# Kernel tuning notes

Measured on AMD Instinct MI355X. Metric: run time of the kernel, lower is better.

## Reference

```python
import jax, jax.numpy as jnp
import numpy as np

NEG_INF_SCALE = -1e9


def setup_inputs() -> dict:
    key = jax.random.key(0)
    ks = jax.random.split(key, 8)
    B, T, M, D = 64, 1024, 256, 1024
    query = jax.random.normal(ks[0], (B, 1, M), dtype=jnp.float32)
    keys = jax.random.normal(ks[1], (B, T, M), dtype=jnp.float32)
    values = jax.random.normal(ks[2], (B, T, D), dtype=jnp.float32)
    mask = jax.random.randint(ks[3], (B, 1, T), 0, 2).astype(jnp.float32)
    # MLP params (scaled like torch default init ~ 1/sqrt(fan_in))
    W1 = jax.random.normal(ks[4], (4 * M, D), dtype=jnp.float32) / np.sqrt(4 * M)
    b1 = jnp.zeros((D,), dtype=jnp.float32)
    W2 = jax.random.normal(ks[5], (D, D), dtype=jnp.float32) / np.sqrt(D)
    b2 = jnp.zeros((D,), dtype=jnp.float32)
    w_score = jax.random.normal(ks[6], (D, 1), dtype=jnp.float32) / np.sqrt(D)
    b_score = jnp.zeros((1,), dtype=jnp.float32)
    return {"query": query, "keys": keys, "values": values, "mask": mask,
            "W1": W1, "b1": b1, "W2": W2, "b2": b2,
            "w_score": w_score, "b_score": b_score}


def reference(query, keys, values, mask, W1, b1, W2, b2, w_score, b_score):
    # query: [B,1,M] broadcast against keys: [B,T,M]
    q = jnp.broadcast_to(query, keys.shape)
    att_input = jnp.concatenate([q, keys, q - keys, q * keys], axis=-1)  # [B,T,4M]
    h = jax.nn.relu(att_input @ W1 + b1)   # [B,T,D]
    h = jax.nn.relu(h @ W2 + b2)           # [B,T,D]
    score = h @ w_score + b_score          # [B,T,1]
    logits = jnp.swapaxes(score, 1, 2)     # [B,1,T]
    logits = logits + mask * NEG_INF_SCALE
    attn = jax.nn.softmax(logits, axis=-1)  # [B,1,T]
    out = jnp.matmul(attn, values)          # [B,1,D]
    return out
```

## Files before the change

### kernel.cpp

```cpp
#include <hip/hip_runtime.h>

#define DEV __device__ __forceinline__

typedef __attribute__((ext_vector_type(4))) float f32x4;
typedef __attribute__((ext_vector_type(8))) short short8;
typedef __attribute__((ext_vector_type(4))) short s16x4;
typedef __attribute__((ext_vector_type(4))) float f32x4v;

DEV short f2bf(float f) {
  union { float f; unsigned u; } v; v.f = f;
  unsigned r = (v.u + 0x7FFFu + ((v.u >> 16) & 1u)) >> 16;
  return (short)r;
}

DEV void gload16(const void* g, void* l) {
  __builtin_amdgcn_global_load_lds(
      (const __attribute__((address_space(1))) void*)g,
      (__attribute__((address_space(3))) void*)l, 16, 0, 0);
}

#define BAR() __builtin_amdgcn_s_barrier()
#define LGKM0()                                          \
  {                                                      \
    asm volatile("s_waitcnt lgkmcnt(0)" ::: "memory");   \
    __builtin_amdgcn_sched_barrier(0);                   \
  }
#define VMW(n)                                                \
  {                                                           \
    asm volatile("s_waitcnt vmcnt(" #n ")" ::: "memory");     \
    __builtin_amdgcn_sched_barrier(0);                        \
  }

#define RD_A(pb, qrt)                                                          \
  _Pragma("unroll") for (int m_ = 0; m_ < 4; ++m_) {                           \
    af[m_][0] = *(const short8*)&lds[(pb) + aoff0 + ((qrt) * 4 + m_) * 1024];  \
    af[m_][1] = *(const short8*)&lds[(pb) + aoff1 + ((qrt) * 4 + m_) * 1024];  \
  }
#define RD_B(pb, nh)                                                             \
  _Pragma("unroll") for (int n_ = 0; n_ < 2; ++n_) {                             \
    bf[nh][n_][0] = *(const short8*)&lds[(pb) + boff0 + ((nh) * 2 + n_) * 1024]; \
    bf[nh][n_][1] = *(const short8*)&lds[(pb) + boff1 + ((nh) * 2 + n_) * 1024]; \
  }
#define MFMA_Q(mq, nh)                                                           \
  __builtin_amdgcn_s_setprio(1);                                                 \
  _Pragma("unroll") for (int m_ = 0; m_ < 4; ++m_) {                             \
    _Pragma("unroll") for (int n_ = 0; n_ < 2; ++n_) {                           \
      acc[(mq) * 4 + m_][(nh) * 2 + n_] =                                        \
          __builtin_amdgcn_mfma_f32_16x16x32_bf16(                               \
              af[m_][0], bf[nh][n_][0], acc[(mq) * 4 + m_][(nh) * 2 + n_], 0, 0, \
              0);                                                                \
      acc[(mq) * 4 + m_][(nh) * 2 + n_] =                                        \
          __builtin_amdgcn_mfma_f32_16x16x32_bf16(                               \
              af[m_][1], bf[nh][n_][1], acc[(mq) * 4 + m_][(nh) * 2 + n_], 0, 0, \
              0);                                                                \
    }                                                                            \
  }                                                                              \
  __builtin_amdgcn_s_setprio(0);

struct FullTag { static constexpr bool value = true; };
struct LastTag { static constexpr bool value = false; };


__global__ __launch_bounds__(256) void k_prep_keys(const float* __restrict__ k,
                                                   short* __restrict__ o) {
  int i = (blockIdx.x * 256 + threadIdx.x) * 8;
  f32x4v v0 = *(const f32x4v*)(k + i);
  f32x4v v1 = *(const f32x4v*)(k + i + 4);
  short8 s;
  s[0] = f2bf(v0[0]); s[1] = f2bf(v0[1]); s[2] = f2bf(v0[2]); s[3] = f2bf(v0[3]);
  s[4] = f2bf(v1[0]); s[5] = f2bf(v1[1]); s[6] = f2bf(v1[2]); s[7] = f2bf(v1[3]);
  *(short8*)(o + i) = s;
}

__global__ __launch_bounds__(256) void k_prep_w2t(const float* __restrict__ w2,
                                                  short* __restrict__ w2t) {
  __shared__ float tile[64][65];
  const int k0 = blockIdx.x * 64, n0 = blockIdx.y * 64;
  const int a = threadIdx.x & 63, q = threadIdx.x >> 6;
#pragma unroll
  for (int i = 0; i < 16; ++i) {
    int kk = i * 4 + q;
    tile[kk][a] = w2[(size_t)(k0 + kk) * 1024 + n0 + a];
  }
  __syncthreads();
#pragma unroll
  for (int i = 0; i < 16; ++i) {
    int nn = i * 4 + q;
    w2t[(size_t)(n0 + nn) * 1024 + k0 + a] = f2bf(tile[a][nn]);
  }
}

__global__ __launch_bounds__(256) void k_prep_wkt(const float* __restrict__ w1,
                                                  const float* __restrict__ query,
                                                  const float* __restrict__ b1,
                                                  short* __restrict__ wkt,
                                                  float* __restrict__ biasb) {
  __shared__ short tile[64][257];
  __shared__ float redm[64][4];
  const int b = blockIdx.x, d0 = blockIdx.y * 64;
  const int d = threadIdx.x & 63, mq = threadIdx.x >> 6;
  float bacc = 0.f;
#pragma unroll 4
  for (int i = 0; i < 64; ++i) {
    int m = i * 4 + mq;
    float qv = query[b * 256 + m];
    float wa = w1[(size_t)m * 1024 + d0 + d];
    float wb = w1[(size_t)(256 + m) * 1024 + d0 + d];
    float wc = w1[(size_t)(512 + m) * 1024 + d0 + d];
    float wd = w1[(size_t)(768 + m) * 1024 + d0 + d];
    tile[d][m] = f2bf(wb - wc + qv * wd);
    bacc += qv * (wa + wc);
  }
  redm[d][mq] = bacc;
  __syncthreads();
  const int m = threadIdx.x;
  for (int dd = 0; dd < 64; ++dd)
    wkt[((size_t)b * 1024 + d0 + dd) * 256 + m] = tile[dd][m];
  if (threadIdx.x < 64) {
    int dd = threadIdx.x;
    biasb[b * 1024 + d0 + dd] =
        redm[dd][0] + redm[dd][1] + redm[dd][2] + redm[dd][3] + b1[d0 + dd];
  }
}


template <int MODE>
__global__ __launch_bounds__(512) void k_gemm8(const short* __restrict__ A,
                                               const short* __restrict__ B,
                                               const float* __restrict__ bias,
                                               const float* __restrict__ wscore,
                                               short* __restrict__ hout,
                                               float* __restrict__ spart) {
  __shared__ short lds[65536];
  constexpr int SK = (MODE == 1) ? 256 : 1024;
  constexpr int KT = (MODE == 1) ? 4 : 16;

  const int tid = threadIdx.x;
  const int bx = blockIdx.x;
  const int L = (bx & 7) * 128 + (bx >> 3);

  const short *Ab, *Bb;
  const float *biasp, *wsp = nullptr;
  short* houtp = nullptr;
  int rt, ct;
  if constexpr (MODE == 1) {
    const int b = L >> 4;
    rt = (L >> 2) & 3; ct = L & 3;
    Ab = A + ((size_t)b * 1024 + rt * 256) * 256;
    Bb = B + ((size_t)b * 1024 + ct * 256) * 256;
    biasp = bias + b * 1024 + ct * 256;
    houtp = hout + ((size_t)(b * 1024 + rt * 256)) * 1024 + ct * 256;
  } else {
    rt = L >> 2; ct = L & 3;
    Ab = A + (size_t)rt * 256 * 1024;
    Bb = B + (size_t)ct * 256 * 1024;
    biasp = bias + ct * 256;
    wsp = wscore + ct * 256;
  }

  const int c0 = tid, c1 = 512 + tid;
  const int r0 = c0 >> 3, k0 = ((c0 & 7) ^ (r0 & 7)) * 8;
  const int r1 = c1 >> 3, k1 = ((c1 & 7) ^ (r1 & 7)) * 8;

  auto STAGE = [&](const short* gb, int kt, int half, int ldsb) {
    gload16(gb + (size_t)(half * 128 + r0) * SK + kt * 64 + k0, &lds[ldsb + c0 * 8]);
    gload16(gb + (size_t)(half * 128 + r1) * SK + kt * 64 + k1, &lds[ldsb + c1 * 8]);
  };

  const int lane = tid & 63, l15 = lane & 15, l4 = lane >> 4;
  const int wid = tid >> 6, wr = wid >> 2, wc = wid & 3;
  const int aoff0 = wr * 8192 + l15 * 64 + ((l4 ^ (l15 & 7)) * 8);
  const int aoff1 = wr * 8192 + l15 * 64 + (((4 + l4) ^ (l15 & 7)) * 8);
  const int boff0 = 16384 + (wc >> 1) * 8192 + (wc & 1) * 4096 + l15 * 64 +
                    ((l4 ^ (l15 & 7)) * 8);
  const int boff1 = 16384 + (wc >> 1) * 8192 + (wc & 1) * 4096 + l15 * 64 +
                    (((4 + l4) ^ (l15 & 7)) * 8);

  f32x4 acc[8][4];
#pragma unroll
  for (int m = 0; m < 8; ++m)
#pragma unroll
    for (int n = 0; n < 4; ++n) acc[m][n] = f32x4{0.f, 0.f, 0.f, 0.f};
  short8 af[4][2];
  short8 bf[2][2][2];

  STAGE(Ab, 0, 0, 0);
  STAGE(Ab, 0, 1, 8192);
  STAGE(Bb, 0, 0, 16384);
  STAGE(Bb, 0, 1, 24576);
  STAGE(Ab, 1, 0, 32768);
  STAGE(Ab, 1, 1, 40960);
  VMW(4);
  BAR();

  auto body = [&](int t, auto tag) {
    constexpr bool FULL = decltype(tag)::value;
    const int p = (t & 1) << 15;
    const int q = p ^ 32768;
    RD_A(p, 0); RD_B(p, 0);
    STAGE(Bb, t + 1, 0, q + 16384);
    BAR(); LGKM0(); MFMA_Q(0, 0); BAR();
    RD_B(p, 1);
    STAGE(Bb, t + 1, 1, q + 24576);
    BAR(); LGKM0(); MFMA_Q(0, 1); BAR();
    RD_A(p, 1);
    if constexpr (FULL) STAGE(Bb, t + 2, 0, p + 16384);
    BAR(); LGKM0(); MFMA_Q(1, 1); BAR();
    if constexpr (FULL) STAGE(Bb, t + 2, 1, p + 24576);
    BAR();
    MFMA_Q(1, 0);
    if constexpr (FULL) { VMW(4); } else { VMW(0); }
    BAR();
    RD_A(q, 0); RD_B(q, 0);
    if constexpr (FULL) STAGE(Ab, t + 2, 0, p + 0);
    BAR(); LGKM0(); MFMA_Q(0, 0); BAR();
    RD_B(q, 1);
    if constexpr (FULL) STAGE(Ab, t + 2, 1, p + 8192);
    BAR(); LGKM0(); MFMA_Q(0, 1); BAR();
    RD_A(q, 1);
    BAR(); LGKM0(); MFMA_Q(1, 1); BAR();
    if constexpr (FULL) { STAGE(Ab, t + 3, 0, q + 0); STAGE(Ab, t + 3, 1, q + 8192); }
    BAR();
    MFMA_Q(1, 0);
    if constexpr (FULL) { VMW(4); }
    BAR();
  };

#pragma nounroll
  for (int i = 0; i < KT / 2 - 1; ++i) body(2 * i, FullTag{});
  body(KT - 2, LastTag{});

  if constexpr (MODE == 1) {
    float bv[4];
#pragma unroll
    for (int n = 0; n < 4; ++n) bv[n] = biasp[wc * 64 + n * 16 + l15];
#pragma unroll
    for (int m = 0; m < 8; ++m) {
#pragma unroll
      for (int r2 = 0; r2 < 4; ++r2) {
        int row = wr * 128 + m * 16 + l4 * 4 + r2;
#pragma unroll
        for (int n = 0; n < 4; ++n) {
          int col = wc * 64 + n * 16 + l15;
          houtp[(size_t)row * 1024 + col] = f2bf(fmaxf(acc[m][n][r2] + bv[n], 0.f));
        }
      }
    }
  } else {
    float bv[4], wv[4];
#pragma unroll
    for (int n = 0; n < 4; ++n) {
      int c = wc * 64 + n * 16 + l15;
      bv[n] = biasp[c];
      wv[n] = wsp[c];
    }
    float* so = spart + ((size_t)(ct * 4 + wc) << 16) + rt * 256 + wr * 128;
#pragma unroll
    for (int m = 0; m < 8; ++m) {
#pragma unroll
      for (int r2 = 0; r2 < 4; ++r2) {
        float s = 0.f;
#pragma unroll
        for (int n = 0; n < 4; ++n) s += fmaxf(acc[m][n][r2] + bv[n], 0.f) * wv[n];
        s += __shfl_xor(s, 1);
        s += __shfl_xor(s, 2);
        s += __shfl_xor(s, 4);
        s += __shfl_xor(s, 8);
        if (l15 == 0) so[m * 16 + l4 * 4 + r2] = s;
      }
    }
  }
}


__global__ __launch_bounds__(256) void k_softmax(const float* __restrict__ spart,
                                                 const float* __restrict__ mask,
                                                 const float* __restrict__ bscore,
                                                 float* __restrict__ attn) {
  const int b = blockIdx.x, tid = threadIdx.x;
  __shared__ float sm[1024];
  __shared__ float red[8];
  const float bs = bscore[0];
  float lmax = -3.0e38f;
  for (int t = tid; t < 1024; t += 256) {
    float s = bs;
#pragma unroll
    for (int c = 0; c < 16; ++c) s += spart[(size_t)c * 65536 + b * 1024 + t];
    float lg = s + mask[b * 1024 + t] * (-1e9f);
    sm[t] = lg;
    lmax = fmaxf(lmax, lg);
  }
  for (int o = 32; o; o >>= 1) lmax = fmaxf(lmax, __shfl_xor(lmax, o));
  const int wid = tid >> 6, lane = tid & 63;
  if (lane == 0) red[wid] = lmax;
  __syncthreads();
  float bmax = fmaxf(fmaxf(red[0], red[1]), fmaxf(red[2], red[3]));
  float lsum = 0.f;
  for (int t = tid; t < 1024; t += 256) {
    float e = __expf(sm[t] - bmax);
    sm[t] = e;
    lsum += e;
  }
  for (int o = 32; o; o >>= 1) lsum += __shfl_xor(lsum, o);
  __syncthreads();
  if (lane == 0) red[wid] = lsum;
  __syncthreads();
  float inv = 1.0f / (red[0] + red[1] + red[2] + red[3]);
  for (int t = tid; t < 1024; t += 256) attn[b * 1024 + t] = sm[t] * inv;
}

__global__ __launch_bounds__(256) void k_out(const float* __restrict__ attn,
                                             const float* __restrict__ values,
                                             float* __restrict__ part) {
  const int b = blockIdx.x >> 3, ts = blockIdx.x & 7;
  const int tid = threadIdx.x;
  __shared__ float at[128];
  if (tid < 128) at[tid] = attn[b * 1024 + ts * 128 + tid];
  __syncthreads();
  const float* vb = values + ((size_t)b * 1024 + ts * 128) * 1024 + tid * 4;
  f32x4 acc = {0.f, 0.f, 0.f, 0.f};
#pragma unroll 8
  for (int t = 0; t < 128; ++t) {
    f32x4v v = *(const f32x4v*)(vb + (size_t)t * 1024);
    float a = at[t];
    acc[0] += a * v[0]; acc[1] += a * v[1]; acc[2] += a * v[2]; acc[3] += a * v[3];
  }
  *(f32x4*)(part + ((size_t)(b * 8 + ts)) * 1024 + tid * 4) = acc;
}

__global__ __launch_bounds__(256) void k_red(const float* __restrict__ part,
                                             float* __restrict__ out) {
  const int b = blockIdx.x;
  const int c4 = threadIdx.x * 4;
  f32x4 s = {0.f, 0.f, 0.f, 0.f};
#pragma unroll
  for (int ts = 0; ts < 8; ++ts) {
    f32x4v v = *(const f32x4v*)(part + ((size_t)(b * 8 + ts)) * 1024 + c4);
    s[0] += v[0]; s[1] += v[1]; s[2] += v[2]; s[3] += v[3];
  }
  *(f32x4*)(out + b * 1024 + c4) = s;
}


extern "C" void kernel_launch(void* const* d_in, const int* in_sizes, int n_in,
                              void* d_out, int out_size, void* d_ws, size_t ws_size,
                              hipStream_t stream) {
  const float* query  = (const float*)d_in[0];
  const float* keys   = (const float*)d_in[1];
  const float* values = (const float*)d_in[2];
  const float* mask   = (const float*)d_in[3];
  const float* W1     = (const float*)d_in[4];
  const float* b1     = (const float*)d_in[5];
  const float* W2     = (const float*)d_in[6];
  const float* b2     = (const float*)d_in[7];
  const float* wscore = (const float*)d_in[8];
  const float* bscore = (const float*)d_in[9];
  float* out = (float*)d_out;

  char* ws = (char*)d_ws;
  short* keysb = (short*)(ws);
  short* wkt   = (short*)(ws + 33554432ull);
  short* w2t   = (short*)(ws + 67108864ull);
  float* biasb = (float*)(ws + 69206016ull);
  short* h1    = (short*)(ws + 69468160ull);
  float* spart = (float*)(ws + 203685888ull);
  float* attn  = (float*)(ws + 207880192ull);
  float* part  = (float*)(ws + 208142336ull);

  k_prep_keys<<<8192, 256, 0, stream>>>(keys, keysb);
  k_prep_w2t<<<dim3(16, 16), 256, 0, stream>>>(W2, w2t);
  k_prep_wkt<<<dim3(64, 16), 256, 0, stream>>>(W1, query, b1, wkt, biasb);

  k_gemm8<1><<<1024, 512, 0, stream>>>(keysb, wkt, biasb, nullptr, h1, nullptr);
  k_gemm8<2><<<1024, 512, 0, stream>>>(h1, w2t, b2, wscore, nullptr, spart);

  k_softmax<<<64, 256, 0, stream>>>(spart, mask, bscore, attn);
  k_out<<<512, 256, 0, stream>>>(attn, values, part);
  k_red<<<64, 256, 0, stream>>>(part, out);
}
```

Measured before the change: 284.4 us.

## Swap MFMA operands for row-major accumulators and batch LDS reads earlier

Swapping the A/B operands of the bf16 MFMA transposes the accumulator layout, so each lane now holds four consecutive columns of one row. The MODE 1 epilogue can then write packed 4-element bf16 stores instead of scalar ones. The score epilogue reduces along the lane's own columns with two cross-lane shuffles instead of four, with bias and weight vectors indexed to match. The main loop also issues the second B-fragment LDS read with the first and uses a partial lgkmcnt wait, so those reads overlap the first MFMA quarter at the cost of more live registers.

```diff
diff --git a/kernel.cpp b/kernel.cpp
--- a/kernel.cpp
+++ b/kernel.cpp
@@ -20,10 +20,10 @@
 }
 
 #define BAR() __builtin_amdgcn_s_barrier()
-#define LGKM0()                                          \
-  {                                                      \
-    asm volatile("s_waitcnt lgkmcnt(0)" ::: "memory");   \
-    __builtin_amdgcn_sched_barrier(0);                   \
+#define LGKMW(n)                                              \
+  {                                                           \
+    asm volatile("s_waitcnt lgkmcnt(" #n ")" ::: "memory");   \
+    __builtin_amdgcn_sched_barrier(0);                        \
   }
 #define VMW(n)                                                \
   {                                                           \
@@ -47,11 +47,11 @@
     _Pragma("unroll") for (int n_ = 0; n_ < 2; ++n_) {                           \
       acc[(mq) * 4 + m_][(nh) * 2 + n_] =                                        \
           __builtin_amdgcn_mfma_f32_16x16x32_bf16(                               \
-              af[m_][0], bf[nh][n_][0], acc[(mq) * 4 + m_][(nh) * 2 + n_], 0, 0, \
+              bf[nh][n_][0], af[m_][0], acc[(mq) * 4 + m_][(nh) * 2 + n_], 0, 0, \
               0);                                                                \
       acc[(mq) * 4 + m_][(nh) * 2 + n_] =                                        \
           __builtin_amdgcn_mfma_f32_16x16x32_bf16(                               \
-              af[m_][1], bf[nh][n_][1], acc[(mq) * 4 + m_][(nh) * 2 + n_], 0, 0, \
+              bf[nh][n_][1], af[m_][1], acc[(mq) * 4 + m_][(nh) * 2 + n_], 0, 0, \
               0);                                                                \
     }                                                                            \
   }                                                                              \
@@ -197,28 +197,26 @@
     constexpr bool FULL = decltype(tag)::value;
     const int p = (t & 1) << 15;
     const int q = p ^ 32768;
-    RD_A(p, 0); RD_B(p, 0);
+    RD_A(p, 0); RD_B(p, 0); RD_B(p, 1);
     STAGE(Bb, t + 1, 0, q + 16384);
-    BAR(); LGKM0(); MFMA_Q(0, 0); BAR();
-    RD_B(p, 1);
+    BAR(); LGKMW(4); MFMA_Q(0, 0); BAR();
     STAGE(Bb, t + 1, 1, q + 24576);
-    BAR(); LGKM0(); MFMA_Q(0, 1); BAR();
+    BAR(); LGKMW(0); MFMA_Q(0, 1); BAR();
     RD_A(p, 1);
     if constexpr (FULL) STAGE(Bb, t + 2, 0, p + 16384);
-    BAR(); LGKM0(); MFMA_Q(1, 1); BAR();
+    BAR(); LGKMW(0); MFMA_Q(1, 1); BAR();
     if constexpr (FULL) STAGE(Bb, t + 2, 1, p + 24576);
     BAR();
     MFMA_Q(1, 0);
     if constexpr (FULL) { VMW(4); } else { VMW(0); }
     BAR();
-    RD_A(q, 0); RD_B(q, 0);
+    RD_A(q, 0); RD_B(q, 0); RD_B(q, 1);
     if constexpr (FULL) STAGE(Ab, t + 2, 0, p + 0);
-    BAR(); LGKM0(); MFMA_Q(0, 0); BAR();
-    RD_B(q, 1);
+    BAR(); LGKMW(4); MFMA_Q(0, 0); BAR();
     if constexpr (FULL) STAGE(Ab, t + 2, 1, p + 8192);
-    BAR(); LGKM0(); MFMA_Q(0, 1); BAR();
+    BAR(); LGKMW(0); MFMA_Q(0, 1); BAR();
     RD_A(q, 1);
-    BAR(); LGKM0(); MFMA_Q(1, 1); BAR();
+    BAR(); LGKMW(0); MFMA_Q(1, 1); BAR();
     if constexpr (FULL) { STAGE(Ab, t + 3, 0, q + 0); STAGE(Ab, t + 3, 1, q + 8192); }
     BAR();
     MFMA_Q(1, 0);
@@ -231,43 +229,45 @@
   body(KT - 2, LastTag{});
 
   if constexpr (MODE == 1) {
-    float bv[4];
-#pragma unroll
-    for (int n = 0; n < 4; ++n) bv[n] = biasp[wc * 64 + n * 16 + l15];
+    float bv[4][4];
+#pragma unroll
+    for (int n = 0; n < 4; ++n)
+#pragma unroll
+      for (int r2 = 0; r2 < 4; ++r2) bv[n][r2] = biasp[wc * 64 + n * 16 + l4 * 4 + r2];
 #pragma unroll
     for (int m = 0; m < 8; ++m) {
-#pragma unroll
-      for (int r2 = 0; r2 < 4; ++r2) {
-        int row = wr * 128 + m * 16 + l4 * 4 + r2;
-#pragma unroll
-        for (int n = 0; n < 4; ++n) {
-          int col = wc * 64 + n * 16 + l15;
-          houtp[(size_t)row * 1024 + col] = f2bf(fmaxf(acc[m][n][r2] + bv[n], 0.f));
-        }
+      int row = wr * 128 + m * 16 + l15;
+#pragma unroll
+      for (int n = 0; n < 4; ++n) {
+        s16x4 pk;
+#pragma unroll
+        for (int r2 = 0; r2 < 4; ++r2)
+          pk[r2] = f2bf(fmaxf(acc[m][n][r2] + bv[n][r2], 0.f));
+        *(s16x4*)&houtp[(size_t)row * 1024 + wc * 64 + n * 16 + l4 * 4] = pk;
       }
     }
   } else {
-    float bv[4], wv[4];
-#pragma unroll
-    for (int n = 0; n < 4; ++n) {
-      int c = wc * 64 + n * 16 + l15;
-      bv[n] = biasp[c];
-      wv[n] = wsp[c];
-    }
+    float bv[4][4], wv[4][4];
+#pragma unroll
+    for (int n = 0; n < 4; ++n)
+#pragma unroll
+      for (int r2 = 0; r2 < 4; ++r2) {
+        int c = wc * 64 + n * 16 + l4 * 4 + r2;
+        bv[n][r2] = biasp[c];
+        wv[n][r2] = wsp[c];
+      }
     float* so = spart + ((size_t)(ct * 4 + wc) << 16) + rt * 256 + wr * 128;
 #pragma unroll
     for (int m = 0; m < 8; ++m) {
-#pragma unroll
-      for (int r2 = 0; r2 < 4; ++r2) {
-        float s = 0.f;
-#pragma unroll
-        for (int n = 0; n < 4; ++n) s += fmaxf(acc[m][n][r2] + bv[n], 0.f) * wv[n];
-        s += __shfl_xor(s, 1);
-        s += __shfl_xor(s, 2);
-        s += __shfl_xor(s, 4);
-        s += __shfl_xor(s, 8);
-        if (l15 == 0) so[m * 16 + l4 * 4 + r2] = s;
-      }
+      float s = 0.f;
+#pragma unroll
+      for (int n = 0; n < 4; ++n)
+#pragma unroll
+        for (int r2 = 0; r2 < 4; ++r2)
+          s += fmaxf(acc[m][n][r2] + bv[n][r2], 0.f) * wv[n][r2];
+      s += __shfl_xor(s, 16);
+      s += __shfl_xor(s, 32);
+      if (lane < 16) so[m * 16 + l15] = s;
     }
   }
 }
```

Result: no change. 282.7 us (-0.6%).
